# Performance work log

Measured on AMD Instinct MI355X. Metric: run time of the kernel, lower is better.

Reference implementation:

```python
import jax, jax.numpy as jnp
import numpy as np

EMBED_DIM = 384
NUM_HEADS = 6
QKV_DIM = EMBED_DIM // 2            # 192
PER_HEAD = QKV_DIM // NUM_HEADS     # 32 (actual head width)
SCALE = (EMBED_DIM // NUM_HEADS) ** -0.5  # uses 64, as in the source


def setup_inputs() -> dict:
    key = jax.random.key(0)
    k1, k2, k3, k4, k5 = jax.random.split(key, 5)
    B, N = 4, 4096
    x = jax.random.normal(k1, (B, N, EMBED_DIM), dtype=jnp.float32)
    # Linear weights stored as [in, out] so y = x @ W + b (equiv. to torch W^T)
    qkv_w = jax.random.normal(k2, (EMBED_DIM, 3 * QKV_DIM), dtype=jnp.float32) * (EMBED_DIM ** -0.5)
    qkv_b = jax.random.normal(k3, (3 * QKV_DIM,), dtype=jnp.float32) * 0.02
    proj_w = jax.random.normal(k4, (QKV_DIM, EMBED_DIM), dtype=jnp.float32) * (QKV_DIM ** -0.5)
    proj_b = jax.random.normal(k5, (EMBED_DIM,), dtype=jnp.float32) * 0.02
    return {"x": x, "qkv_w": qkv_w, "qkv_b": qkv_b, "proj_w": proj_w, "proj_b": proj_b}


def reference(x, qkv_w, qkv_b, proj_w, proj_b):
    B, N, C = x.shape
    qkv = x @ qkv_w + qkv_b                                  # [B,N,3*192]
    qkv = qkv.reshape(B, N, 3, NUM_HEADS, PER_HEAD)
    qkv = jnp.transpose(qkv, (2, 0, 3, 1, 4))                # [3,B,H,N,d]
    q, k, v = qkv[0], qkv[1], qkv[2]
    attn = jnp.einsum('bhnd,bhmd->bhnm', q, k) * SCALE       # [B,H,N,N]
    attn = jax.nn.softmax(attn, axis=-1)                     # dropout: eval mode (identity)
    out = jnp.einsum('bhnm,bhmd->bhnd', attn, v)             # [B,H,N,d]
    out = jnp.transpose(out, (0, 2, 1, 3)).reshape(B, N, QKV_DIM)
    return out @ proj_w + proj_b                             # [B,N,384]
```

## Files before the change

### kernel.cpp

```cpp
#include <hip/hip_runtime.h>

typedef __attribute__((ext_vector_type(8))) short short8;
typedef __attribute__((ext_vector_type(2))) float f32x2;
typedef __attribute__((ext_vector_type(4))) float f32x4;
typedef __attribute__((ext_vector_type(16))) float f32x16;
typedef __attribute__((ext_vector_type(4))) unsigned short u16x4;
typedef __attribute__((ext_vector_type(2))) unsigned int u32x2;
typedef __attribute__((ext_vector_type(4))) unsigned int u32x4;

#define LOG2E 1.4426950408889634f

static __device__ __forceinline__ float fexp2(float x) {
  float r;
  asm("v_exp_f32 %0, %1" : "=v"(r) : "v"(x));
  return r;
}

static __device__ __forceinline__ unsigned short f2bf(float f) {
  unsigned int u = __float_as_uint(f);
  u += 0x7fffu + ((u >> 16) & 1u);
  return (unsigned short)(u >> 16);
}

static __device__ __forceinline__ void swap32(unsigned& a, unsigned& b) {
#if __has_builtin(__builtin_amdgcn_permlane32_swap)
  u32x2 r = __builtin_amdgcn_permlane32_swap(a, b, false, false);
  a = r.x; b = r.y;
#else
  unsigned pa = (unsigned)__shfl_xor((int)a, 32);
  unsigned pb = (unsigned)__shfl_xor((int)b, 32);
  bool hi = (threadIdx.x & 32) != 0;
  unsigned na = hi ? pb : a;
  unsigned nb = hi ? b : pa;
  a = na; b = nb;
#endif
}

__global__ void k_cast(const float* __restrict__ x, unsigned short* __restrict__ xb,
                       const float* __restrict__ wq, const float* __restrict__ wp,
                       unsigned short* __restrict__ wqt, unsigned short* __restrict__ wpt) {
  if (blockIdx.x < 6144) {
    int i = blockIdx.x * blockDim.x + threadIdx.x;
    float4 v = reinterpret_cast<const float4*>(x)[i];
    u16x4 o;
    o.x = f2bf(v.x); o.y = f2bf(v.y); o.z = f2bf(v.z); o.w = f2bf(v.w);
    reinterpret_cast<u16x4*>(xb)[i] = o;
  } else {
    int i = (blockIdx.x - 6144) * blockDim.x + threadIdx.x;
    if (i < 221184) {
      int c = i / 384, k = i % 384;
      wqt[i] = f2bf(wq[k * 576 + c]);
    } else {
      int j = i - 221184;
      int c = j / 192, k = j % 192;
      wpt[j] = f2bf(wp[k * 384 + c]);
    }
  }
}

__global__ __launch_bounds__(256) void k_qkv(const unsigned short* __restrict__ xb,
                                             const unsigned short* __restrict__ wt,
                                             const float* __restrict__ bias,
                                             unsigned short* __restrict__ Qb,
                                             unsigned short* __restrict__ Kb,
                                             unsigned short* __restrict__ Vt) {
  int w = threadIdx.x >> 6, lane = threadIdx.x & 63;
  int l31 = lane & 31, h1 = lane >> 5;
  int cg = blockIdx.x >> 6;
  int rb = blockIdx.x & 63;
  int r0 = rb * 256 + w * 64;
  int c0 = cg * 64;
  int b_ = r0 >> 12, n0 = r0 & 4095;

  const unsigned short* xa = xb + (r0 + l31) * 384 + h1 * 8;
  const unsigned short* wa = wt + (c0 + l31) * 384 + h1 * 8;

  f32x16 acc[2][2] = {};

  if (cg < 6) {
#pragma unroll 4
    for (int t = 0; t < 24; ++t) {
      short8 x0 = *reinterpret_cast<const short8*>(xa + t * 16);
      short8 x1 = *reinterpret_cast<const short8*>(xa + 12288 + t * 16);
      short8 w0 = *reinterpret_cast<const short8*>(wa + t * 16);
      short8 w1 = *reinterpret_cast<const short8*>(wa + 12288 + t * 16);
      acc[0][0] = __builtin_amdgcn_mfma_f32_32x32x16_bf16(x0, w0, acc[0][0], 0, 0, 0);
      acc[0][1] = __builtin_amdgcn_mfma_f32_32x32x16_bf16(x0, w1, acc[0][1], 0, 0, 0);
      acc[1][0] = __builtin_amdgcn_mfma_f32_32x32x16_bf16(x1, w0, acc[1][0], 0, 0, 0);
      acc[1][1] = __builtin_amdgcn_mfma_f32_32x32x16_bf16(x1, w1, acc[1][1], 0, 0, 0);
    }
#pragma unroll
    for (int Cs = 0; Cs < 2; ++Cs) {
      int colbase = c0 + Cs * 32;
      int which = colbase / 192;
      int h = (colbase % 192) / 32;
      int bh = b_ * 6 + h;
      float bv = bias[colbase + l31];
      unsigned short* dstb = (which == 0 ? Qb : Kb) + (unsigned)bh * 4096 * 32 + l31;
#pragma unroll
      for (int Rs = 0; Rs < 2; ++Rs) {
#pragma unroll
        for (int r = 0; r < 16; ++r) {
          int n = n0 + Rs * 32 + (r & 3) + 8 * (r >> 2) + 4 * h1;
          float v = acc[Rs][Cs][r] + bv;
          if (which == 0) v *= (0.125f * LOG2E);
          dstb[n * 32] = f2bf(v);
        }
      }
    }
  } else {
#pragma unroll 4
    for (int t = 0; t < 24; ++t) {
      short8 x0 = *reinterpret_cast<const short8*>(xa + t * 16);
      short8 x1 = *reinterpret_cast<const short8*>(xa + 12288 + t * 16);
      short8 w0 = *reinterpret_cast<const short8*>(wa + t * 16);
      short8 w1 = *reinterpret_cast<const short8*>(wa + 12288 + t * 16);
      acc[0][0] = __builtin_amdgcn_mfma_f32_32x32x16_bf16(w0, x0, acc[0][0], 0, 0, 0);
      acc[0][1] = __builtin_amdgcn_mfma_f32_32x32x16_bf16(w1, x0, acc[0][1], 0, 0, 0);
      acc[1][0] = __builtin_amdgcn_mfma_f32_32x32x16_bf16(w0, x1, acc[1][0], 0, 0, 0);
      acc[1][1] = __builtin_amdgcn_mfma_f32_32x32x16_bf16(w1, x1, acc[1][1], 0, 0, 0);
    }
    int rem0 = c0 - 384;
#pragma unroll
    for (int Cs = 0; Cs < 2; ++Cs) {
      int rem = rem0 + Cs * 32;
      int h = rem / 32;
      int bh = b_ * 6 + h;
#pragma unroll
      for (int r = 0; r < 16; ++r) {
        int dreg = (r & 3) + 8 * (r >> 2) + 4 * h1;
        float bv = bias[384 + rem + dreg];
#pragma unroll
        for (int Rs = 0; Rs < 2; ++Rs) {
          int n = n0 + Rs * 32 + l31;
          Vt[((unsigned)bh * 32 + dreg) * 4096 + n] = f2bf(acc[Rs][Cs][r] + bv);
        }
      }
    }
  }
}

__global__ __launch_bounds__(256) void k_attn(const unsigned short* __restrict__ Qb,
                                              const unsigned short* __restrict__ Kb,
                                              const unsigned short* __restrict__ Vt,
                                              unsigned short* __restrict__ AO) {
  __shared__ __align__(16) unsigned short sm[16384];
  char* kbp = (char*)sm;
  char* vbp = (char*)sm + 8192;

  int tid = threadIdx.x;
  int lane = tid & 63, w = tid >> 6;
  int l31 = lane & 31, h1 = lane >> 5;
  int lb = (blockIdx.x & 7) * 96 + (blockIdx.x >> 3);
  int bh = lb >> 5, qt = lb & 31;
  int b_ = bh / 6, h = bh % 6;
  int qb = qt * 128 + w * 32;

  const unsigned short* Qp = Qb + (bh * 4096 + qb) * 32;
  short8 q0 = *reinterpret_cast<const short8*>(Qp + l31 * 32 + h1 * 8);
  short8 q1 = *reinterpret_cast<const short8*>(Qp + l31 * 32 + 16 + h1 * 8);

  const unsigned short* Kbh = Kb + bh * 4096 * 32;
  const unsigned short* Vbh = Vt + bh * 32 * 4096;
  int krow = tid >> 2;
  int kslot = (tid & 3) ^ ((krow >> 1) & 3);
  const unsigned short* gk = Kbh + krow * 32 + kslot * 8;
  int vrow = tid >> 4;
  int vslot = (tid & 15) ^ (vrow & 7);
  const unsigned short* gv = Vbh + vrow * 4096 + vslot * 8;
  int dst = tid * 16;

  int ak0 = l31 * 64 + ((h1 ^ ((l31 >> 1) & 3)) << 4);
  int ak1 = ak0 ^ 32;
  int av0 = l31 * 256 + (((0 + h1) ^ (l31 & 7)) << 4);
  int av1 = l31 * 256 + (((2 + h1) ^ (l31 & 7)) << 4);
  int av2 = l31 * 256 + (((4 + h1) ^ (l31 & 7)) << 4);
  int av3 = l31 * 256 + (((6 + h1) ^ (l31 & 7)) << 4);

  f32x16 o = {};
  f32x2 lacc = {0.f, 0.f};
  short8 rk0, rk1, rv0, rv1;

#define STAGE_LOAD(T)                                                            \
  do {                                                                           \
    rk0 = *reinterpret_cast<const short8*>(gk + (T) * 4096);                     \
    rk1 = *reinterpret_cast<const short8*>(gk + (T) * 4096 + 2048);              \
    rv0 = *reinterpret_cast<const short8*>(gv + (T) * 128);                      \
    rv1 = *reinterpret_cast<const short8*>(gv + (T) * 128 + 65536);              \
  } while (0)

#define STAGE_WRITE(BO)                                                          \
  do {                                                                           \
    *reinterpret_cast<short8*>(kbp + (BO) + dst) = rk0;                          \
    *reinterpret_cast<short8*>(kbp + (BO) + dst + 4096) = rk1;                   \
    *reinterpret_cast<short8*>(vbp + (BO) + dst) = rv0;                          \
    *reinterpret_cast<short8*>(vbp + (BO) + dst + 4096) = rv1;                   \
  } while (0)

#define COMP(BO, U)                                                              \
  do {                                                                           \
    short8 K0 = *reinterpret_cast<const short8*>(kbp + (BO) + (U) * 4096 + ak0); \
    short8 K1 = *reinterpret_cast<const short8*>(kbp + (BO) + (U) * 4096 + ak1); \
    short8 K2 = *reinterpret_cast<const short8*>(kbp + (BO) + (U) * 4096 + 2048 + ak0); \
    short8 K3 = *reinterpret_cast<const short8*>(kbp + (BO) + (U) * 4096 + 2048 + ak1); \
    short8 V0 = *reinterpret_cast<const short8*>(vbp + (BO) + (U) * 128 + av0);  \
    short8 V1 = *reinterpret_cast<const short8*>(vbp + (BO) + (U) * 128 + av1);  \
    short8 V2 = *reinterpret_cast<const short8*>(vbp + (BO) + (U) * 128 + av2);  \
    short8 V3 = *reinterpret_cast<const short8*>(vbp + (BO) + (U) * 128 + av3);  \
    f32x16 z_ = {};                                                              \
    __builtin_amdgcn_s_setprio(1);                                               \
    f32x16 sA = __builtin_amdgcn_mfma_f32_32x32x16_bf16(K0, q0, z_, 0, 0, 0);    \
    sA = __builtin_amdgcn_mfma_f32_32x32x16_bf16(K1, q1, sA, 0, 0, 0);           \
    f32x16 sB = __builtin_amdgcn_mfma_f32_32x32x16_bf16(K2, q0, z_, 0, 0, 0);    \
    sB = __builtin_amdgcn_mfma_f32_32x32x16_bf16(K3, q1, sB, 0, 0, 0);           \
    __builtin_amdgcn_s_setprio(0);                                               \
    float pA[16], pB[16];                                                        \
    _Pragma("unroll") for (int i = 0; i < 16; ++i) pA[i] = fexp2(sA[i]);         \
    _Pragma("unroll") for (int i = 0; i < 16; ++i) pB[i] = fexp2(sB[i]);         \
    _Pragma("unroll") for (int i = 0; i < 8; ++i) {                              \
      f32x2 a_ = {pA[2 * i], pA[2 * i + 1]};                                     \
      f32x2 b_ = {pB[2 * i], pB[2 * i + 1]};                                     \
      lacc += a_ + b_;                                                           \
    }                                                                            \
    unsigned w0, w1, w2, w3, w4, w5, w6, w7;                                     \
    asm("v_cvt_pk_bf16_f32 %0, %1, %2" : "=v"(w0) : "v"(pA[0]), "v"(pA[1]));     \
    asm("v_cvt_pk_bf16_f32 %0, %1, %2" : "=v"(w1) : "v"(pA[2]), "v"(pA[3]));     \
    asm("v_cvt_pk_bf16_f32 %0, %1, %2" : "=v"(w2) : "v"(pA[4]), "v"(pA[5]));     \
    asm("v_cvt_pk_bf16_f32 %0, %1, %2" : "=v"(w3) : "v"(pA[6]), "v"(pA[7]));     \
    asm("v_cvt_pk_bf16_f32 %0, %1, %2" : "=v"(w4) : "v"(pA[8]), "v"(pA[9]));     \
    asm("v_cvt_pk_bf16_f32 %0, %1, %2" : "=v"(w5) : "v"(pA[10]), "v"(pA[11]));   \
    asm("v_cvt_pk_bf16_f32 %0, %1, %2" : "=v"(w6) : "v"(pA[12]), "v"(pA[13]));   \
    asm("v_cvt_pk_bf16_f32 %0, %1, %2" : "=v"(w7) : "v"(pA[14]), "v"(pA[15]));   \
    swap32(w0, w2); swap32(w1, w3); swap32(w4, w6); swap32(w5, w7);              \
    u32x4 pa0v = {w0, w1, w2, w3};                                               \
    u32x4 pa1v = {w4, w5, w6, w7};                                               \
    unsigned y0, y1, y2, y3, y4, y5, y6, y7;                                     \
    asm("v_cvt_pk_bf16_f32 %0, %1, %2" : "=v"(y0) : "v"(pB[0]), "v"(pB[1]));     \
    asm("v_cvt_pk_bf16_f32 %0, %1, %2" : "=v"(y1) : "v"(pB[2]), "v"(pB[3]));     \
    asm("v_cvt_pk_bf16_f32 %0, %1, %2" : "=v"(y2) : "v"(pB[4]), "v"(pB[5]));     \
    asm("v_cvt_pk_bf16_f32 %0, %1, %2" : "=v"(y3) : "v"(pB[6]), "v"(pB[7]));     \
    asm("v_cvt_pk_bf16_f32 %0, %1, %2" : "=v"(y4) : "v"(pB[8]), "v"(pB[9]));     \
    asm("v_cvt_pk_bf16_f32 %0, %1, %2" : "=v"(y5) : "v"(pB[10]), "v"(pB[11]));   \
    asm("v_cvt_pk_bf16_f32 %0, %1, %2" : "=v"(y6) : "v"(pB[12]), "v"(pB[13]));   \
    asm("v_cvt_pk_bf16_f32 %0, %1, %2" : "=v"(y7) : "v"(pB[14]), "v"(pB[15]));   \
    swap32(y0, y2); swap32(y1, y3); swap32(y4, y6); swap32(y5, y7);              \
    u32x4 pb0v = {y0, y1, y2, y3};                                               \
    u32x4 pb1v = {y4, y5, y6, y7};                                               \
    __builtin_amdgcn_s_setprio(1);                                               \
    o = __builtin_amdgcn_mfma_f32_32x32x16_bf16(V0, __builtin_bit_cast(short8, pa0v), o, 0, 0, 0); \
    o = __builtin_amdgcn_mfma_f32_32x32x16_bf16(V1, __builtin_bit_cast(short8, pa1v), o, 0, 0, 0); \
    o = __builtin_amdgcn_mfma_f32_32x32x16_bf16(V2, __builtin_bit_cast(short8, pb0v), o, 0, 0, 0); \
    o = __builtin_amdgcn_mfma_f32_32x32x16_bf16(V3, __builtin_bit_cast(short8, pb1v), o, 0, 0, 0); \
    __builtin_amdgcn_s_setprio(0);                                               \
  } while (0)

  STAGE_LOAD(0);
  STAGE_WRITE(0);
  __syncthreads();

#pragma unroll 1
  for (int tt = 0; tt < 16; ++tt) {
    STAGE_LOAD(2 * tt + 1);
    COMP(0, 0);
    STAGE_WRITE(16384);
    COMP(0, 1);
    __syncthreads();
    if (tt < 15) STAGE_LOAD(2 * tt + 2);
    COMP(16384, 0);
    if (tt < 15) STAGE_WRITE(0);
    COMP(16384, 1);
    __syncthreads();
  }
#undef STAGE_LOAD
#undef STAGE_WRITE
#undef COMP

  float l = lacc.x + lacc.y;
  l += __shfl_xor(l, 32);
  float inv = 1.0f / l;
  unsigned short* aop = AO + (b_ * 4096 + qb + l31) * 192 + h * 32 + h1 * 4;
#pragma unroll
  for (int qd = 0; qd < 4; ++qd) {
    u16x4 st;
    st.x = f2bf(o[qd * 4 + 0] * inv);
    st.y = f2bf(o[qd * 4 + 1] * inv);
    st.z = f2bf(o[qd * 4 + 2] * inv);
    st.w = f2bf(o[qd * 4 + 3] * inv);
    *reinterpret_cast<u16x4*>(aop + qd * 8) = st;
  }
}

__global__ __launch_bounds__(256) void k_proj(const unsigned short* __restrict__ AO,
                                              const unsigned short* __restrict__ wt,
                                              const float* __restrict__ bias,
                                              float* __restrict__ out) {
  int w = threadIdx.x >> 6, lane = threadIdx.x & 63;
  int l31 = lane & 31, h1 = lane >> 5;
  int cg = blockIdx.x >> 6;
  int rb = blockIdx.x & 63;
  int r0 = rb * 256 + w * 64;
  int c0 = cg * 64;

  const unsigned short* aa = AO + (r0 + l31) * 192 + h1 * 8;
  const unsigned short* wa = wt + (c0 + l31) * 192 + h1 * 8;

  f32x16 acc[2][2] = {};
#pragma unroll 4
  for (int t = 0; t < 12; ++t) {
    short8 a0 = *reinterpret_cast<const short8*>(aa + t * 16);
    short8 a1 = *reinterpret_cast<const short8*>(aa + 6144 + t * 16);
    short8 w0 = *reinterpret_cast<const short8*>(wa + t * 16);
    short8 w1 = *reinterpret_cast<const short8*>(wa + 6144 + t * 16);
    acc[0][0] = __builtin_amdgcn_mfma_f32_32x32x16_bf16(a0, w0, acc[0][0], 0, 0, 0);
    acc[0][1] = __builtin_amdgcn_mfma_f32_32x32x16_bf16(a0, w1, acc[0][1], 0, 0, 0);
    acc[1][0] = __builtin_amdgcn_mfma_f32_32x32x16_bf16(a1, w0, acc[1][0], 0, 0, 0);
    acc[1][1] = __builtin_amdgcn_mfma_f32_32x32x16_bf16(a1, w1, acc[1][1], 0, 0, 0);
  }
#pragma unroll
  for (int Cs = 0; Cs < 2; ++Cs) {
    int col = c0 + Cs * 32 + l31;
    float bv = bias[col];
#pragma unroll
    for (int Rs = 0; Rs < 2; ++Rs) {
#pragma unroll
      for (int r = 0; r < 16; ++r) {
        int n = r0 + Rs * 32 + (r & 3) + 8 * (r >> 2) + 4 * h1;
        out[n * 384 + col] = acc[Rs][Cs][r] + bv;
      }
    }
  }
}

extern "C" void kernel_launch(void* const* d_in, const int* in_sizes, int n_in,
                              void* d_out, int out_size, void* d_ws, size_t ws_size,
                              hipStream_t stream) {
  const float* x      = (const float*)d_in[0];
  const float* qkv_w  = (const float*)d_in[1];
  const float* qkv_b  = (const float*)d_in[2];
  const float* proj_w = (const float*)d_in[3];
  const float* proj_b = (const float*)d_in[4];
  float* out = (float*)d_out;
  char* ws = (char*)d_ws;

  unsigned short* xb    = (unsigned short*)(ws);
  unsigned short* wqkvt = (unsigned short*)(ws + 12582912);
  unsigned short* wpt   = (unsigned short*)(ws + 13025280);
  unsigned short* Qb    = (unsigned short*)(ws + 13172736);
  unsigned short* Kb    = (unsigned short*)(ws + 19464192);
  unsigned short* Vt    = (unsigned short*)(ws + 25755648);
  unsigned short* AO    = (unsigned short*)(ws + 32047104);

  k_cast <<<7296, 256, 0, stream>>>(x, xb, qkv_w, proj_w, wqkvt, wpt);
  k_qkv  <<< 576, 256, 0, stream>>>(xb, wqkvt, qkv_b, Qb, Kb, Vt);
  k_attn <<< 768, 256, 0, stream>>>(Qb, Kb, Vt, AO);
  k_proj <<< 384, 256, 0, stream>>>(AO, wpt, proj_b, out);
}
```

Before: 149.4 us.

## Software-pipeline QK and PV MFMAs with exp/convert chunks across sub-tiles

Restructures the attention inner loop so each staged tile handles both sub-tiles together. The QK MFMAs of the second sub-tile, and then the PV MFMAs of the first, are interleaved with the exp2, bf16-pack and row-sum work in 8-element chunks. The goal is to hide VALU/transcendental latency behind matrix-core work instead of running them serially. The setprio hints are dropped, and more live registers (two sets of scores and packed probabilities) may raise register pressure.

```diff
diff --git a/kernel.cpp b/kernel.cpp
--- a/kernel.cpp
+++ b/kernel.cpp
@@ -197,61 +197,74 @@
     *reinterpret_cast<short8*>(vbp + (BO) + dst + 4096) = rv1;                   \
   } while (0)
 
-#define COMP(BO, U)                                                              \
+#define CHUNK(S, B, OUT)                                                         \
   do {                                                                           \
-    short8 K0 = *reinterpret_cast<const short8*>(kbp + (BO) + (U) * 4096 + ak0); \
-    short8 K1 = *reinterpret_cast<const short8*>(kbp + (BO) + (U) * 4096 + ak1); \
-    short8 K2 = *reinterpret_cast<const short8*>(kbp + (BO) + (U) * 4096 + 2048 + ak0); \
-    short8 K3 = *reinterpret_cast<const short8*>(kbp + (BO) + (U) * 4096 + 2048 + ak1); \
-    short8 V0 = *reinterpret_cast<const short8*>(vbp + (BO) + (U) * 128 + av0);  \
-    short8 V1 = *reinterpret_cast<const short8*>(vbp + (BO) + (U) * 128 + av1);  \
-    short8 V2 = *reinterpret_cast<const short8*>(vbp + (BO) + (U) * 128 + av2);  \
-    short8 V3 = *reinterpret_cast<const short8*>(vbp + (BO) + (U) * 128 + av3);  \
+    float p0 = fexp2(S[(B) + 0]), p1 = fexp2(S[(B) + 1]);                        \
+    float p2 = fexp2(S[(B) + 2]), p3 = fexp2(S[(B) + 3]);                        \
+    float p4 = fexp2(S[(B) + 4]), p5 = fexp2(S[(B) + 5]);                        \
+    float p6 = fexp2(S[(B) + 6]), p7 = fexp2(S[(B) + 7]);                        \
+    unsigned c0, c1, c2, c3;                                                     \
+    asm("v_cvt_pk_bf16_f32 %0, %1, %2" : "=v"(c0) : "v"(p0), "v"(p1));           \
+    asm("v_cvt_pk_bf16_f32 %0, %1, %2" : "=v"(c1) : "v"(p2), "v"(p3));           \
+    asm("v_cvt_pk_bf16_f32 %0, %1, %2" : "=v"(c2) : "v"(p4), "v"(p5));           \
+    asm("v_cvt_pk_bf16_f32 %0, %1, %2" : "=v"(c3) : "v"(p6), "v"(p7));           \
+    swap32(c0, c2); swap32(c1, c3);                                              \
+    u32x4 t_ = {c0, c1, c2, c3};                                                 \
+    OUT = __builtin_bit_cast(short8, t_);                                        \
+    f32x2 x01 = {p0, p1}, x23 = {p2, p3}, x45 = {p4, p5}, x67 = {p6, p7};        \
+    lacc += (x01 + x23) + (x45 + x67);                                           \
+  } while (0)
+
+#define TILE(BO, WBO, T, DO)                                                     \
+  do {                                                                           \
+    if (DO) STAGE_LOAD(T);                                                       \
+                                                              \
+    short8 K0 = *reinterpret_cast<const short8*>(kbp + (BO) + ak0);              \
+    short8 K1 = *reinterpret_cast<const short8*>(kbp + (BO) + ak1);              \
+    short8 K2 = *reinterpret_cast<const short8*>(kbp + (BO) + 2048 + ak0);       \
+    short8 K3 = *reinterpret_cast<const short8*>(kbp + (BO) + 2048 + ak1);       \
     f32x16 z_ = {};                                                              \
-    __builtin_amdgcn_s_setprio(1);                                               \
-    f32x16 sA = __builtin_amdgcn_mfma_f32_32x32x16_bf16(K0, q0, z_, 0, 0, 0);    \
-    sA = __builtin_amdgcn_mfma_f32_32x32x16_bf16(K1, q1, sA, 0, 0, 0);           \
-    f32x16 sB = __builtin_amdgcn_mfma_f32_32x32x16_bf16(K2, q0, z_, 0, 0, 0);    \
-    sB = __builtin_amdgcn_mfma_f32_32x32x16_bf16(K3, q1, sB, 0, 0, 0);           \
-    __builtin_amdgcn_s_setprio(0);                                               \
-    float pA[16], pB[16];                                                        \
-    _Pragma("unroll") for (int i = 0; i < 16; ++i) pA[i] = fexp2(sA[i]);         \
-    _Pragma("unroll") for (int i = 0; i < 16; ++i) pB[i] = fexp2(sB[i]);         \
-    _Pragma("unroll") for (int i = 0; i < 8; ++i) {                              \
-      f32x2 a_ = {pA[2 * i], pA[2 * i + 1]};                                     \
-      f32x2 b_ = {pB[2 * i], pB[2 * i + 1]};                                     \
-      lacc += a_ + b_;                                                           \
-    }                                                                            \
-    unsigned w0, w1, w2, w3, w4, w5, w6, w7;                                     \
-    asm("v_cvt_pk_bf16_f32 %0, %1, %2" : "=v"(w0) : "v"(pA[0]), "v"(pA[1]));     \
-    asm("v_cvt_pk_bf16_f32 %0, %1, %2" : "=v"(w1) : "v"(pA[2]), "v"(pA[3]));     \
-    asm("v_cvt_pk_bf16_f32 %0, %1, %2" : "=v"(w2) : "v"(pA[4]), "v"(pA[5]));     \
-    asm("v_cvt_pk_bf16_f32 %0, %1, %2" : "=v"(w3) : "v"(pA[6]), "v"(pA[7]));     \
-    asm("v_cvt_pk_bf16_f32 %0, %1, %2" : "=v"(w4) : "v"(pA[8]), "v"(pA[9]));     \
-    asm("v_cvt_pk_bf16_f32 %0, %1, %2" : "=v"(w5) : "v"(pA[10]), "v"(pA[11]));   \
-    asm("v_cvt_pk_bf16_f32 %0, %1, %2" : "=v"(w6) : "v"(pA[12]), "v"(pA[13]));   \
-    asm("v_cvt_pk_bf16_f32 %0, %1, %2" : "=v"(w7) : "v"(pA[14]), "v"(pA[15]));   \
-    swap32(w0, w2); swap32(w1, w3); swap32(w4, w6); swap32(w5, w7);              \
-    u32x4 pa0v = {w0, w1, w2, w3};                                               \
-    u32x4 pa1v = {w4, w5, w6, w7};                                               \
-    unsigned y0, y1, y2, y3, y4, y5, y6, y7;                                     \
-    asm("v_cvt_pk_bf16_f32 %0, %1, %2" : "=v"(y0) : "v"(pB[0]), "v"(pB[1]));     \
-    asm("v_cvt_pk_bf16_f32 %0, %1, %2" : "=v"(y1) : "v"(pB[2]), "v"(pB[3]));     \
-    asm("v_cvt_pk_bf16_f32 %0, %1, %2" : "=v"(y2) : "v"(pB[4]), "v"(pB[5]));     \
-    asm("v_cvt_pk_bf16_f32 %0, %1, %2" : "=v"(y3) : "v"(pB[6]), "v"(pB[7]));     \
-    asm("v_cvt_pk_bf16_f32 %0, %1, %2" : "=v"(y4) : "v"(pB[8]), "v"(pB[9]));     \
-    asm("v_cvt_pk_bf16_f32 %0, %1, %2" : "=v"(y5) : "v"(pB[10]), "v"(pB[11]));   \
-    asm("v_cvt_pk_bf16_f32 %0, %1, %2" : "=v"(y6) : "v"(pB[12]), "v"(pB[13]));   \
-    asm("v_cvt_pk_bf16_f32 %0, %1, %2" : "=v"(y7) : "v"(pB[14]), "v"(pB[15]));   \
-    swap32(y0, y2); swap32(y1, y3); swap32(y4, y6); swap32(y5, y7);              \
-    u32x4 pb0v = {y0, y1, y2, y3};                                               \
-    u32x4 pb1v = {y4, y5, y6, y7};                                               \
-    __builtin_amdgcn_s_setprio(1);                                               \
-    o = __builtin_amdgcn_mfma_f32_32x32x16_bf16(V0, __builtin_bit_cast(short8, pa0v), o, 0, 0, 0); \
-    o = __builtin_amdgcn_mfma_f32_32x32x16_bf16(V1, __builtin_bit_cast(short8, pa1v), o, 0, 0, 0); \
-    o = __builtin_amdgcn_mfma_f32_32x32x16_bf16(V2, __builtin_bit_cast(short8, pb0v), o, 0, 0, 0); \
-    o = __builtin_amdgcn_mfma_f32_32x32x16_bf16(V3, __builtin_bit_cast(short8, pb1v), o, 0, 0, 0); \
-    __builtin_amdgcn_s_setprio(0);                                               \
+    f32x16 sA0 = __builtin_amdgcn_mfma_f32_32x32x16_bf16(K0, q0, z_, 0, 0, 0);   \
+    sA0 = __builtin_amdgcn_mfma_f32_32x32x16_bf16(K1, q1, sA0, 0, 0, 0);         \
+    f32x16 sB0 = __builtin_amdgcn_mfma_f32_32x32x16_bf16(K2, q0, z_, 0, 0, 0);   \
+    sB0 = __builtin_amdgcn_mfma_f32_32x32x16_bf16(K3, q1, sB0, 0, 0, 0);         \
+                                    \
+    short8 K4 = *reinterpret_cast<const short8*>(kbp + (BO) + 4096 + ak0);       \
+    short8 K5 = *reinterpret_cast<const short8*>(kbp + (BO) + 4096 + ak1);       \
+    short8 K6 = *reinterpret_cast<const short8*>(kbp + (BO) + 6144 + ak0);       \
+    short8 K7 = *reinterpret_cast<const short8*>(kbp + (BO) + 6144 + ak1);       \
+    short8 pa0, pa1, pa2, pa3, pb0, pb1, pb2, pb3;                               \
+    f32x16 sA1 = __builtin_amdgcn_mfma_f32_32x32x16_bf16(K4, q0, z_, 0, 0, 0);   \
+    CHUNK(sA0, 0, pa0);                                                          \
+    sA1 = __builtin_amdgcn_mfma_f32_32x32x16_bf16(K5, q1, sA1, 0, 0, 0);         \
+    CHUNK(sA0, 8, pa1);                                                          \
+    f32x16 sB1 = __builtin_amdgcn_mfma_f32_32x32x16_bf16(K6, q0, z_, 0, 0, 0);   \
+    CHUNK(sB0, 0, pa2);                                                          \
+    sB1 = __builtin_amdgcn_mfma_f32_32x32x16_bf16(K7, q1, sB1, 0, 0, 0);         \
+    CHUNK(sB0, 8, pa3);                                                          \
+    if (DO) STAGE_WRITE(WBO);                                                    \
+                                    \
+    short8 V0 = *reinterpret_cast<const short8*>(vbp + (BO) + av0);              \
+    short8 V1 = *reinterpret_cast<const short8*>(vbp + (BO) + av1);              \
+    short8 V2 = *reinterpret_cast<const short8*>(vbp + (BO) + av2);              \
+    short8 V3 = *reinterpret_cast<const short8*>(vbp + (BO) + av3);              \
+    o = __builtin_amdgcn_mfma_f32_32x32x16_bf16(V0, pa0, o, 0, 0, 0);            \
+    CHUNK(sA1, 0, pb0);                                                          \
+    o = __builtin_amdgcn_mfma_f32_32x32x16_bf16(V1, pa1, o, 0, 0, 0);            \
+    CHUNK(sA1, 8, pb1);                                                          \
+    o = __builtin_amdgcn_mfma_f32_32x32x16_bf16(V2, pa2, o, 0, 0, 0);            \
+    CHUNK(sB1, 0, pb2);                                                          \
+    o = __builtin_amdgcn_mfma_f32_32x32x16_bf16(V3, pa3, o, 0, 0, 0);            \
+    CHUNK(sB1, 8, pb3);                                                          \
+                                                              \
+    short8 V4 = *reinterpret_cast<const short8*>(vbp + (BO) + 128 + av0);        \
+    short8 V5 = *reinterpret_cast<const short8*>(vbp + (BO) + 128 + av1);        \
+    short8 V6 = *reinterpret_cast<const short8*>(vbp + (BO) + 128 + av2);        \
+    short8 V7 = *reinterpret_cast<const short8*>(vbp + (BO) + 128 + av3);        \
+    o = __builtin_amdgcn_mfma_f32_32x32x16_bf16(V4, pb0, o, 0, 0, 0);            \
+    o = __builtin_amdgcn_mfma_f32_32x32x16_bf16(V5, pb1, o, 0, 0, 0);            \
+    o = __builtin_amdgcn_mfma_f32_32x32x16_bf16(V6, pb2, o, 0, 0, 0);            \
+    o = __builtin_amdgcn_mfma_f32_32x32x16_bf16(V7, pb3, o, 0, 0, 0);            \
   } while (0)
 
   STAGE_LOAD(0);
@@ -260,20 +273,15 @@
 
 #pragma unroll 1
   for (int tt = 0; tt < 16; ++tt) {
-    STAGE_LOAD(2 * tt + 1);
-    COMP(0, 0);
-    STAGE_WRITE(16384);
-    COMP(0, 1);
+    TILE(0, 16384, 2 * tt + 1, 1);
     __syncthreads();
-    if (tt < 15) STAGE_LOAD(2 * tt + 2);
-    COMP(16384, 0);
-    if (tt < 15) STAGE_WRITE(0);
-    COMP(16384, 1);
+    TILE(16384, 0, 2 * tt + 2, (tt < 15));
     __syncthreads();
   }
 #undef STAGE_LOAD
 #undef STAGE_WRITE
-#undef COMP
+#undef CHUNK
+#undef TILE
 
   float l = lacc.x + lacc.y;
   l += __shfl_xor(l, 32);
```

Measured after the change: 146.4 us. 2.0% less time.
